# Optimization experiments

Measured on AMD Instinct MI355X. Metric: run time of the kernel, lower is better.

## Reference

```python
import jax, jax.numpy as jnp
import numpy as np

D, H, L, P, NQ, B, DFF = 256, 8, 4, 5, 900, 8, 1024
DH = D // H
SHAPES = np.array([[128, 128], [64, 64], [32, 32], [16, 16]], dtype=np.int64)
S = int((SHAPES[:, 0] * SHAPES[:, 1]).sum())  # 21760
EPS = 1e-5


def layer_norm(x, g, b):
    m = jnp.mean(x, -1, keepdims=True)
    v = jnp.mean((x - m) ** 2, -1, keepdims=True)
    return (x - m) * jax.lax.rsqrt(v + EPS) * g + b


def bilerp(v2, x, y, Wl, Hl):
    # v2: [BH, Hl, Wl, Dh]; x, y: [BH, N] pixel coords (align_corners=False)
    x0 = jnp.floor(x); y0 = jnp.floor(y)
    fx = x - x0; fy = y - y0
    x0i = x0.astype(jnp.int32); y0i = y0.astype(jnp.int32)
    bidx = jnp.arange(v2.shape[0])[:, None]
    out = jnp.zeros(x.shape + (v2.shape[-1],), v2.dtype)
    for dy in (0, 1):
        for dx in (0, 1):
            xi = x0i + dx; yi = y0i + dy
            w = (fx if dx else 1.0 - fx) * (fy if dy else 1.0 - fy)
            valid = (xi >= 0) & (xi < Wl) & (yi >= 0) & (yi < Hl)
            xc = jnp.clip(xi, 0, Wl - 1); yc = jnp.clip(yi, 0, Hl - 1)
            out = out + (w * valid)[..., None] * v2[bidx, yc, xc]
    return out


def setup_inputs() -> dict:
    key = jax.random.key(0)
    ks = jax.random.split(key, 32)
    p = lambda i, shp: (jax.random.normal(ks[i], shp, jnp.float32) * 0.02)
    inp = {
        'tgt': jax.random.normal(ks[0], (NQ, B, D), jnp.float32),
        'tgt_query_pos': jax.random.normal(ks[1], (NQ, B, D), jnp.float32),
        'tgt_reference_points': jax.random.uniform(ks[2], (NQ, B, L, 4), jnp.float32),
        'memory': jax.random.normal(ks[3], (S, B, D), jnp.float32),
        'sa_in_w': p(4, (3 * D, D)), 'sa_in_b': jnp.zeros((3 * D,)),
        'sa_out_w': p(5, (D, D)), 'sa_out_b': jnp.zeros((D,)),
        'off_w': p(6, (H * L * P * 2, D)), 'off_b': jax.random.uniform(ks[7], (H * L * P * 2,), jnp.float32, -1.0, 1.0),
        'aw_w': p(8, (H * L * P, D)), 'aw_b': jnp.zeros((H * L * P,)),
        'val_w': p(9, (D, D)), 'val_b': jnp.zeros((D,)),
        'co_w': p(10, (D, D)), 'co_b': jnp.zeros((D,)),
        'w1': p(11, (DFF, D)), 'b1': jnp.zeros((DFF,)),
        'w2': p(12, (D, DFF)), 'b2': jnp.zeros((D,)),
        'ln1_g': jnp.ones((D,)), 'ln1_b': jnp.zeros((D,)),
        'ln2_g': jnp.ones((D,)), 'ln2_b': jnp.zeros((D,)),
        'ln3_g': jnp.ones((D,)), 'ln3_b': jnp.zeros((D,)),
        'memory_spatial_shapes': np.array(SHAPES),
        'memory_level_start_index': np.concatenate([[0], np.cumsum(SHAPES[:, 0] * SHAPES[:, 1])[:-1]]),
    }
    return inp


def reference(tgt, tgt_query_pos, tgt_reference_points, memory,
              sa_in_w, sa_in_b, sa_out_w, sa_out_b,
              off_w, off_b, aw_w, aw_b, val_w, val_b, co_w, co_b,
              w1, b1, w2, b2, ln1_g, ln1_b, ln2_g, ln2_b, ln3_g, ln3_b,
              memory_spatial_shapes, memory_level_start_index):
    shapes = np.asarray(memory_spatial_shapes)

    # ---- self-attention (norm2) ----
    q = tgt + tgt_query_pos  # [nq,B,D], k == q, v == tgt
    qp = (q @ sa_in_w[:D].T + sa_in_b[:D]).reshape(NQ, B, H, DH)
    kp = (q @ sa_in_w[D:2 * D].T + sa_in_b[D:2 * D]).reshape(NQ, B, H, DH)
    vp = (tgt @ sa_in_w[2 * D:].T + sa_in_b[2 * D:]).reshape(NQ, B, H, DH)
    scores = jnp.einsum('qbhd,kbhd->bhqk', qp, kp) / jnp.sqrt(jnp.float32(DH))
    attn = jax.nn.softmax(scores, -1)
    sa = jnp.einsum('bhqk,kbhd->qbhd', attn, vp).reshape(NQ, B, D)
    sa = sa @ sa_out_w.T + sa_out_b
    tgt = layer_norm(tgt + sa, ln2_g, ln2_b)

    # ---- deformable cross-attention (norm1) ----
    query = (tgt + tgt_query_pos).transpose(1, 0, 2)          # [B,nq,D]
    value = (memory.transpose(1, 0, 2) @ val_w.T + val_b).reshape(B, S, H, DH)
    offsets = (query @ off_w.T + off_b).reshape(B, NQ, H, L, P, 2)
    aw = (query @ aw_w.T + aw_b).reshape(B, NQ, H, L * P)
    aw = jax.nn.softmax(aw, -1).reshape(B, NQ, H, L, P)
    ref = tgt_reference_points.transpose(1, 0, 2, 3)          # [B,nq,L,4]
    locs = ref[:, :, None, :, None, :2] + offsets / P * ref[:, :, None, :, None, 2:] * 0.5

    acc = jnp.zeros((B, H, NQ, DH), jnp.float32)
    start = 0
    for l in range(L):
        Hl, Wl = int(shapes[l, 0]), int(shapes[l, 1])
        v2 = value[:, start:start + Hl * Wl].reshape(B, Hl, Wl, H, DH)
        v2 = v2.transpose(0, 3, 1, 2, 4).reshape(B * H, Hl, Wl, DH)
        loc = locs[:, :, :, l].transpose(0, 2, 1, 3, 4).reshape(B * H, NQ * P, 2)
        x = loc[..., 0] * Wl - 0.5
        y = loc[..., 1] * Hl - 0.5
        samp = bilerp(v2, x, y, Wl, Hl).reshape(B, H, NQ, P, DH)
        w_l = aw[:, :, :, l].transpose(0, 2, 1, 3)            # [B,H,nq,P]
        acc = acc + jnp.einsum('bhqp,bhqpd->bhqd', w_l, samp)
        start += Hl * Wl
    ca = acc.transpose(0, 2, 1, 3).reshape(B, NQ, D) @ co_w.T + co_b
    tgt = layer_norm(tgt + ca.transpose(1, 0, 2), ln1_g, ln1_b)

    # ---- FFN (norm3) ----
    h = jax.nn.relu(tgt @ w1.T + b1) @ w2.T + b2
    tgt = layer_norm(tgt + h, ln3_g, ln3_b)
    return tgt
```

## Files before the change

### kernel.cpp

```cpp
#include <hip/hip_runtime.h>
#include <hip/hip_bf16.h>

#define NQ   900
#define BB   8
#define DD   256
#define HH   8
#define DH   32
#define LL   4
#define PP   5
#define SS   21760
#define DFF  1024
#define MQ   (NQ*BB)
#define MV   (SS*BB)

typedef __bf16 bf16_t;
typedef __bf16 bf16x8 __attribute__((ext_vector_type(8)));
typedef __bf16 bf16x4 __attribute__((ext_vector_type(4)));
typedef float  f32x4  __attribute__((ext_vector_type(4)));

__device__ __forceinline__ void async16(const void* g, void* l) {
  __builtin_amdgcn_global_load_lds(
      (const __attribute__((address_space(1))) unsigned int*)g,
      (__attribute__((address_space(3))) unsigned int*)l, 16, 0, 0);
}

template<typename AT, typename OT, int RELU>
__global__ __launch_bounds__(256) void vgemm(
    const AT* __restrict__ A, const bf16_t* __restrict__ W,
    const float* __restrict__ bias, OT* __restrict__ C,
    int M, int N, int nt)
{
  constexpr bool AF = (sizeof(AT) == 4);
  __shared__ __align__(16) bf16_t Ws[64 * 256];
  const int blk = blockIdx.x;
  const int tn = blk % nt, tm = blk / nt;
  const int n0 = tn << 6, m0 = tm << 8;
  const int t = threadIdx.x, wave = t >> 6, lane = t & 63;
  const int lm = lane & 15, quad = lane >> 4;

#pragma unroll
  for (int j = 0; j < 8; ++j) {
    int flat = j * 4096 + t * 16;
    int col = flat >> 9;
    int kc = ((flat >> 4) & 31) ^ (col & 31);
    int colg = n0 + col; if (colg >= N) colg = N - 1;
    async16(&W[(size_t)colg * 256 + kc * 8], (char*)Ws + flat);
  }
  __syncthreads();

  f32x4 acc[4][4];
#pragma unroll
  for (int i = 0; i < 4; ++i)
#pragma unroll
    for (int j = 0; j < 4; ++j) acc[i][j] = (f32x4){0.f, 0.f, 0.f, 0.f};

#pragma unroll 2
  for (int k0 = 0; k0 < 256; k0 += 32) {
    const int ki = k0 >> 3;
    bf16x8 bfr[4];
#pragma unroll
    for (int ni = 0; ni < 4; ++ni) {
      int col = ni * 16 + lm;
      int ch = (ki + quad) ^ (col & 31);
      bfr[ni] = *(const bf16x8*)&Ws[col * 256 + ch * 8];
    }
    bf16x8 af[4];
#pragma unroll
    for (int mi = 0; mi < 4; ++mi) {
      int row = m0 + wave * 64 + mi * 16 + lm; if (row >= M) row = M - 1;
      if constexpr (AF) {
        const float* ap = A + (size_t)row * 256 + k0 + quad * 8;
        f32x4 lo = *(const f32x4*)ap;
        f32x4 hi = *(const f32x4*)(ap + 4);
        bf16x8 f;
#pragma unroll
        for (int j = 0; j < 4; ++j) { f[j] = (bf16_t)lo[j]; f[4 + j] = (bf16_t)hi[j]; }
        af[mi] = f;
      } else {
        af[mi] = *(const bf16x8*)&A[(size_t)row * 256 + k0 + quad * 8];
      }
    }
#pragma unroll
    for (int mi = 0; mi < 4; ++mi)
#pragma unroll
      for (int ni = 0; ni < 4; ++ni)
        acc[mi][ni] = __builtin_amdgcn_mfma_f32_16x16x32_bf16(af[mi], bfr[ni], acc[mi][ni], 0, 0, 0);
  }

  float bv[4];
#pragma unroll
  for (int ni = 0; ni < 4; ++ni) {
    int c = n0 + ni * 16 + lm;
    bv[ni] = (c < N) ? bias[c] : 0.f;
  }

  if constexpr (sizeof(OT) == 4) {
#pragma unroll
    for (int mi = 0; mi < 4; ++mi) {
#pragma unroll
      for (int r = 0; r < 4; ++r) {
        int row = m0 + wave * 64 + mi * 16 + quad * 4 + r;
        if (row < M) {
#pragma unroll
          for (int ni = 0; ni < 4; ++ni) {
            int col = n0 + ni * 16 + lm;
            if (col < N) {
              float v = acc[mi][ni][r] + bv[ni];
              if (RELU) v = fmaxf(v, 0.f);
              C[(size_t)row * N + col] = (OT)v;
            }
          }
        }
      }
    }
  } else {
    __syncthreads();
    bf16_t* Os = Ws;
#pragma unroll
    for (int mi = 0; mi < 4; ++mi)
#pragma unroll
      for (int r = 0; r < 4; ++r) {
        int rl = wave * 64 + mi * 16 + quad * 4 + r;
#pragma unroll
        for (int ni = 0; ni < 4; ++ni) {
          float v = acc[mi][ni][r] + bv[ni];
          if (RELU) v = fmaxf(v, 0.f);
          Os[rl * 64 + ni * 16 + lm] = (bf16_t)v;
        }
      }
    __syncthreads();
#pragma unroll
    for (int i = 0; i < 8; ++i) {
      int fe = i * 2048 + t * 8;
      int rl = fe >> 6, cl = fe & 63;
      int row = m0 + rl, colg = n0 + cl;
      if (row < M && colg < N)
        *(bf16x8*)&C[(size_t)row * N + colg] = *(const bf16x8*)&Os[fe];
    }
  }
}

template<typename AT, int EPI, typename OT>
__global__ __launch_bounds__(256) void gemm128(
    const AT* __restrict__ A, const bf16_t* __restrict__ W,
    const float* __restrict__ bias, OT* __restrict__ C,
    int M, int N, int K, int tiles_n)
{
  __shared__ __align__(16) bf16_t As[128 * 32];
  __shared__ __align__(16) bf16_t Bs[128 * 32];
  const int tm = blockIdx.x / tiles_n;
  const int tn = blockIdx.x - tm * tiles_n;
  const int m0 = tm << 7, n0 = tn << 7;
  const int t = threadIdx.x;
  const int wave = t >> 6, lane = t & 63;
  const int wr = wave >> 1, wc = wave & 1;
  const int lm = lane & 15, kq = lane >> 4;

  f32x4 acc[4][4];
#pragma unroll
  for (int i = 0; i < 4; ++i)
#pragma unroll
    for (int j = 0; j < 4; ++j) acc[i][j] = (f32x4){0.f, 0.f, 0.f, 0.f};

  for (int k0 = 0; k0 < K; k0 += 32) {
    __syncthreads();
#pragma unroll
    for (int i = 0; i < 2; ++i) {
      int flat = i * 4096 + t * 16;
      int row = flat >> 6;
      int cl = (flat >> 4) & 3;
      int cg = cl ^ ((row >> 1) & 3);
      int grow = m0 + row; if (grow >= M) grow = M - 1;
      async16(&A[(size_t)grow * K + k0 + cg * 8], (char*)As + flat);
    }
#pragma unroll
    for (int i = 0; i < 2; ++i) {
      int flat = i * 4096 + t * 16;
      int row = flat >> 6;
      int cl = (flat >> 4) & 3;
      int cg = cl ^ ((row >> 1) & 3);
      int grow = n0 + row; if (grow >= N) grow = N - 1;
      async16(&W[(size_t)grow * K + k0 + cg * 8], (char*)Bs + flat);
    }
    __syncthreads();

    bf16x8 af[4], bfr[4];
#pragma unroll
    for (int mi = 0; mi < 4; ++mi) {
      int row = wr * 64 + mi * 16 + lm;
      int s = (row >> 1) & 3;
      af[mi] = *(const bf16x8*)((const bf16_t*)As + row * 32 + ((kq ^ s) << 3));
    }
#pragma unroll
    for (int ni = 0; ni < 4; ++ni) {
      int row = wc * 64 + ni * 16 + lm;
      int s = (row >> 1) & 3;
      bfr[ni] = *(const bf16x8*)(Bs + row * 32 + ((kq ^ s) << 3));
    }
#pragma unroll
    for (int mi = 0; mi < 4; ++mi)
#pragma unroll
      for (int ni = 0; ni < 4; ++ni)
        acc[mi][ni] = __builtin_amdgcn_mfma_f32_16x16x32_bf16(af[mi], bfr[ni], acc[mi][ni], 0, 0, 0);
  }

  const int colb = n0 + wc * 64 + lm;
  float bv[4]; bool cok[4];
#pragma unroll
  for (int ni = 0; ni < 4; ++ni) {
    int c = colb + ni * 16;
    cok[ni] = (c < N);
    bv[ni] = cok[ni] ? bias[c] : 0.f;
  }
#pragma unroll
  for (int mi = 0; mi < 4; ++mi) {
    int rbase = m0 + wr * 64 + mi * 16 + kq * 4;
#pragma unroll
    for (int reg = 0; reg < 4; ++reg) {
      int r = rbase + reg;
      if (r < M) {
#pragma unroll
        for (int ni = 0; ni < 4; ++ni) if (cok[ni]) {
          float v = acc[mi][ni][reg] + bv[ni];
          if (EPI == 1) v = fmaxf(v, 0.f);
          C[(size_t)r * N + colb + ni * 16] = (OT)v;
        }
      }
    }
  }
}

__global__ __launch_bounds__(256) void cvt_all(
    const float* __restrict__ s0, const float* __restrict__ s1,
    const float* __restrict__ s2, const float* __restrict__ s3,
    const float* __restrict__ s4, const float* __restrict__ s5,
    const float* __restrict__ s6, const float* __restrict__ s7,
    bf16_t* __restrict__ dst)
{
  int i = blockIdx.x * 256 + threadIdx.x;
  if (i >= 130048) return;
  const float* s; int base;
  if (i < 24576)      { s = s0; base = 0; }
  else if (i < 32768) { s = s1; base = 24576; }
  else if (i < 43008) { s = s2; base = 32768; }
  else if (i < 48128) { s = s3; base = 43008; }
  else if (i < 56320) { s = s4; base = 48128; }
  else if (i < 64512) { s = s5; base = 56320; }
  else if (i < 97280) { s = s6; base = 64512; }
  else                { s = s7; base = 97280; }
  int li = i - base;
  f32x4 x0 = ((const f32x4*)s)[2 * li], x1 = ((const f32x4*)s)[2 * li + 1];
  bf16x8 r;
#pragma unroll
  for (int j = 0; j < 4; ++j) { r[j] = (bf16_t)x0[j]; r[4 + j] = (bf16_t)x1[j]; }
  ((bf16x8*)dst)[i] = r;
}

__global__ __launch_bounds__(256) void addpos_kernel(
    const float* __restrict__ a, const float* __restrict__ b,
    bf16_t* __restrict__ o, int n8)
{
  int i = blockIdx.x * 256 + threadIdx.x;
  if (i < n8) {
    f32x4 x0 = ((const f32x4*)a)[2 * i], x1 = ((const f32x4*)a)[2 * i + 1];
    f32x4 y0 = ((const f32x4*)b)[2 * i], y1 = ((const f32x4*)b)[2 * i + 1];
    bf16x8 r;
#pragma unroll
    for (int j = 0; j < 4; ++j) { r[j] = (bf16_t)(x0[j] + y0[j]); r[4 + j] = (bf16_t)(x1[j] + y1[j]); }
    ((bf16x8*)o)[i] = r;
  }
}

template<int WBF>
__global__ __launch_bounds__(256) void lnres_kernel(
    const float* __restrict__ x, const float* __restrict__ res,
    const float* __restrict__ g, const float* __restrict__ bta,
    float* __restrict__ out, bf16_t* __restrict__ outb, int rows)
{
  int wave = threadIdx.x >> 6, lane = threadIdx.x & 63;
  int row = blockIdx.x * 4 + wave;
  if (row >= rows) return;
  const float4* xp = (const float4*)(x + (size_t)row * DD);
  const float4* rp = (const float4*)(res + (size_t)row * DD);
  float4 v = xp[lane], rr = rp[lane];
  float a0 = v.x + rr.x, a1 = v.y + rr.y, a2 = v.z + rr.z, a3 = v.w + rr.w;
  float s = a0 + a1 + a2 + a3;
#pragma unroll
  for (int off = 32; off; off >>= 1) s += __shfl_xor(s, off);
  float mean = s * (1.0f / DD);
  float d0 = a0 - mean, d1 = a1 - mean, d2 = a2 - mean, d3 = a3 - mean;
  float vs = d0 * d0 + d1 * d1 + d2 * d2 + d3 * d3;
#pragma unroll
  for (int off = 32; off; off >>= 1) vs += __shfl_xor(vs, off);
  float inv = rsqrtf(vs * (1.0f / DD) + 1e-5f);
  float4 gg = ((const float4*)g)[lane];
  float4 bb = ((const float4*)bta)[lane];
  float o0 = d0 * inv * gg.x + bb.x, o1 = d1 * inv * gg.y + bb.y;
  float o2 = d2 * inv * gg.z + bb.z, o3 = d3 * inv * gg.w + bb.w;
  float4 o; o.x = o0; o.y = o1; o.z = o2; o.w = o3;
  ((float4*)(out + (size_t)row * DD))[lane] = o;
  if (WBF) {
    bf16x4 ob; ob[0] = (bf16_t)o0; ob[1] = (bf16_t)o1; ob[2] = (bf16_t)o2; ob[3] = (bf16_t)o3;
    ((bf16x4*)(outb + (size_t)row * DD))[lane] = ob;
  }
}

__global__ __launch_bounds__(256) void attn_mfma(
    const bf16_t* __restrict__ qk, const bf16_t* __restrict__ vp,
    bf16_t* __restrict__ sa)
{
  __shared__ __align__(16) bf16_t Ks[128 * 32];
  __shared__ __align__(16) bf16_t VT[32 * 136];
  __shared__ __align__(16) bf16_t Pw[4][16 * 136];
  const int bh = blockIdx.x;
  const int b = bh & 7, h = bh >> 3;
  const int qt = blockIdx.y;
  const int t = threadIdx.x, wave = t >> 6, lane = t & 63;
  const int lm = lane & 15, quad = lane >> 4;
  const int q0 = qt * 64 + wave * 16;

  int qrow = q0 + lm; if (qrow > NQ - 1) qrow = NQ - 1;
  bf16x8 aqr = *(const bf16x8*)&qk[((size_t)qrow * BB + b) * 512 + h * 32 + quad * 8];
  bf16x8 aq;
#pragma unroll
  for (int j = 0; j < 8; ++j) aq[j] = (bf16_t)((float)aqr[j] * 0.17677669529663687f);

  f32x4 m_run = {-1e30f, -1e30f, -1e30f, -1e30f};
  f32x4 l_run = {0.f, 0.f, 0.f, 0.f};
  f32x4 o0 = {0.f, 0.f, 0.f, 0.f}, o1 = {0.f, 0.f, 0.f, 0.f};
  const f32x4 zero = {0.f, 0.f, 0.f, 0.f};

  for (int c = 0; c < 8; ++c) {
    const int k0 = c * 128;
    __syncthreads();
#pragma unroll
    for (int i = 0; i < 2; ++i) {
      int flat = i * 4096 + t * 16;
      int row = flat >> 6;
      int cl = (flat >> 4) & 3;
      int cg = cl ^ ((row >> 1) & 3);
      int key = k0 + row; if (key > NQ - 1) key = NQ - 1;
      async16(&qk[((size_t)key * BB + b) * 512 + 256 + h * 32 + cg * 8], (char*)Ks + flat);
    }
#pragma unroll
    for (int i = 0; i < 2; ++i) {
      int idx = t * 2 + i;
      int key = idx >> 2, dc = idx & 3;
      int gk = k0 + key;
      if (gk < NQ) {
        bf16x8 vv = *(const bf16x8*)&vp[((size_t)gk * BB + b) * 256 + h * 32 + dc * 8];
#pragma unroll
        for (int u = 0; u < 8; ++u) VT[(dc * 8 + u) * 136 + key] = vv[u];
      } else {
#pragma unroll
        for (int u = 0; u < 8; ++u) VT[(dc * 8 + u) * 136 + key] = (bf16_t)0.f;
      }
    }
    __syncthreads();

    f32x4 s[8];
#pragma unroll
    for (int blk = 0; blk < 8; ++blk) {
      int row = blk * 16 + lm;
      int sw = (row >> 1) & 3;
      bf16x8 kb = *(const bf16x8*)&Ks[row * 32 + ((quad ^ sw) << 3)];
      s[blk] = __builtin_amdgcn_mfma_f32_16x16x32_bf16(aq, kb, zero, 0, 0, 0);
    }
    if (c == 7) {
#pragma unroll
      for (int blk = 0; blk < 8; ++blk) {
        if (k0 + blk * 16 + lm >= NQ) {
#pragma unroll
          for (int r = 0; r < 4; ++r) s[blk][r] = -1e30f;
        }
      }
    }
    f32x4 mx = s[0];
#pragma unroll
    for (int blk = 1; blk < 8; ++blk)
#pragma unroll
      for (int r = 0; r < 4; ++r) mx[r] = fmaxf(mx[r], s[blk][r]);
#pragma unroll
    for (int d = 1; d < 16; d <<= 1)
#pragma unroll
      for (int r = 0; r < 4; ++r) mx[r] = fmaxf(mx[r], __shfl_xor(mx[r], d));
    f32x4 m_new, alpha;
#pragma unroll
    for (int r = 0; r < 4; ++r) {
      m_new[r] = fmaxf(m_run[r], mx[r]);
      alpha[r] = __expf(m_run[r] - m_new[r]);
    }
    f32x4 psum = {0.f, 0.f, 0.f, 0.f};
#pragma unroll
    for (int blk = 0; blk < 8; ++blk) {
#pragma unroll
      for (int r = 0; r < 4; ++r) {
        float p = __expf(s[blk][r] - m_new[r]);
        psum[r] += p;
        Pw[wave][(quad * 4 + r) * 136 + blk * 16 + lm] = (bf16_t)p;
      }
    }
#pragma unroll
    for (int d = 1; d < 16; d <<= 1)
#pragma unroll
      for (int r = 0; r < 4; ++r) psum[r] += __shfl_xor(psum[r], d);
#pragma unroll
    for (int r = 0; r < 4; ++r) {
      l_run[r] = l_run[r] * alpha[r] + psum[r];
      m_run[r] = m_new[r];
      o0[r] *= alpha[r];
      o1[r] *= alpha[r];
    }
    bf16x8 ap[4];
#pragma unroll
    for (int kc = 0; kc < 4; ++kc)
      ap[kc] = *(const bf16x8*)&Pw[wave][lm * 136 + kc * 32 + quad * 8];
#pragma unroll
    for (int kc = 0; kc < 4; ++kc) {
      bf16x8 vb0 = *(const bf16x8*)&VT[lm * 136 + kc * 32 + quad * 8];
      bf16x8 vb1 = *(const bf16x8*)&VT[(16 + lm) * 136 + kc * 32 + quad * 8];
      o0 = __builtin_amdgcn_mfma_f32_16x16x32_bf16(ap[kc], vb0, o0, 0, 0, 0);
      o1 = __builtin_amdgcn_mfma_f32_16x16x32_bf16(ap[kc], vb1, o1, 0, 0, 0);
    }
  }
#pragma unroll
  for (int r = 0; r < 4; ++r) {
    int q = q0 + quad * 4 + r;
    if (q < NQ) {
      float inv = 1.0f / l_run[r];
      size_t base = ((size_t)q * BB + b) * 256 + h * 32;
      sa[base + lm] = (bf16_t)(o0[r] * inv);
      sa[base + 16 + lm] = (bf16_t)(o1[r] * inv);
    }
  }
}

__global__ __launch_bounds__(256) void deform_kernel(
    const bf16_t* __restrict__ value, const float* __restrict__ offs,
    const float* __restrict__ awl, const float* __restrict__ refp,
    bf16_t* __restrict__ out)
{
  __shared__ float logits[160];
  __shared__ float wfin[160][4];
  __shared__ int   tidx[160][4];
  __shared__ float hmax[8], hsum[8];
  const int r = blockIdx.x;
  const int b = r & 7;
  const int t = threadIdx.x;
  if (t < 160) {
    int i20 = t % 20;
    int l = i20 / 5;
    logits[t] = awl[(size_t)r * 160 + t];
    float ox = offs[(size_t)r * 320 + t * 2];
    float oy = offs[(size_t)r * 320 + t * 2 + 1];
    const float* rp = refp + ((size_t)r * LL + l) * 4;
    int Wl = 128 >> l;
    int st = (l == 0) ? 0 : (l == 1) ? 16384 : (l == 2) ? 20480 : 21504;
    float lx = rp[0] + ox * 0.1f * rp[2];
    float ly = rp[1] + oy * 0.1f * rp[3];
    float xx = lx * (float)Wl - 0.5f;
    float yy = ly * (float)Wl - 0.5f;
    float x0f = floorf(xx), y0f = floorf(yy);
    float fx = xx - x0f, fy = yy - y0f;
    int x0 = (int)x0f, y0 = (int)y0f;
#pragma unroll
    for (int tap = 0; tap < 4; ++tap) {
      int dx = tap & 1, dy = tap >> 1;
      int xi = x0 + dx, yi = y0 + dy;
      float w = (dx ? fx : 1.0f - fx) * (dy ? fy : 1.0f - fy);
      bool valid = (xi >= 0) & (xi < Wl) & (yi >= 0) & (yi < Wl);
      int xc = min(max(xi, 0), Wl - 1);
      int yc = min(max(yi, 0), Wl - 1);
      tidx[t][tap] = (st + yc * Wl + xc) * BB + b;
      wfin[t][tap] = valid ? w : 0.0f;
    }
  }
  __syncthreads();
  if (t < 8) {
    float m = -1e30f;
    for (int i = 0; i < 20; ++i) m = fmaxf(m, logits[t * 20 + i]);
    float s = 0.f;
    for (int i = 0; i < 20; ++i) s += __expf(logits[t * 20 + i] - m);
    hmax[t] = m; hsum[t] = s;
  }
  __syncthreads();
  if (t < 160) {
    int h = t / 20;
    float p = __expf(logits[t] - hmax[h]) / hsum[h];
#pragma unroll
    for (int tap = 0; tap < 4; ++tap) wfin[t][tap] *= p;
  }
  __syncthreads();
  const int h = t >> 5, d = t & 31;
  const bf16_t* vbase = value + h * 32 + d;
  float acc = 0.f;
#pragma unroll 4
  for (int i = 0; i < 20; ++i) {
    int e = h * 20 + i;
#pragma unroll
    for (int tap = 0; tap < 4; ++tap) {
      float w = wfin[e][tap];
      float v = (float)vbase[(size_t)tidx[e][tap] * 256];
      acc = fmaf(w, v, acc);
    }
  }
  out[(size_t)r * 256 + t] = (bf16_t)acc;
}

static inline int tiles(int x) { return (x + 127) >> 7; }

extern "C" void kernel_launch(void* const* d_in, const int* in_sizes, int n_in,
                              void* d_out, int out_size, void* d_ws, size_t ws_size,
                              hipStream_t stream) {
  const float* tgt     = (const float*)d_in[0];
  const float* pos     = (const float*)d_in[1];
  const float* refp    = (const float*)d_in[2];
  const float* memory  = (const float*)d_in[3];
  const float* sa_in_w = (const float*)d_in[4];
  const float* sa_in_b = (const float*)d_in[5];
  const float* sa_out_w= (const float*)d_in[6];
  const float* sa_out_b= (const float*)d_in[7];
  const float* off_w   = (const float*)d_in[8];
  const float* off_b   = (const float*)d_in[9];
  const float* aw_w    = (const float*)d_in[10];
  const float* aw_b    = (const float*)d_in[11];
  const float* val_w   = (const float*)d_in[12];
  const float* val_b   = (const float*)d_in[13];
  const float* co_w    = (const float*)d_in[14];
  const float* co_b    = (const float*)d_in[15];
  const float* w1      = (const float*)d_in[16];
  const float* b1      = (const float*)d_in[17];
  const float* w2      = (const float*)d_in[18];
  const float* b2      = (const float*)d_in[19];
  const float* ln1_g   = (const float*)d_in[20];
  const float* ln1_b   = (const float*)d_in[21];
  const float* ln2_g   = (const float*)d_in[22];
  const float* ln2_b   = (const float*)d_in[23];
  const float* ln3_g   = (const float*)d_in[24];
  const float* ln3_b   = (const float*)d_in[25];

  char* ws = (char*)d_ws;
  bf16_t* value_bf = (bf16_t*)ws;
  bf16_t* qk_bf    = (bf16_t*)(ws + 89128960);
  bf16_t* h1_bf    = qk_bf;
  bf16_t* qsum_bf  = (bf16_t*)(ws + 103874560);
  bf16_t* vp_bf    = (bf16_t*)(ws + 107560960);
  bf16_t* sa_bf    = (bf16_t*)(ws + 111247360);
  float*  tgt2     = (float*)(ws + 114933760);
  bf16_t* query_bf = (bf16_t*)(ws + 122306560);
  float*  offs     = (float*)(ws + 125992960);
  float*  awl      = (float*)(ws + 135208960);
  bf16_t* ca_bf    = (bf16_t*)(ws + 139816960);
  float*  gout     = (float*)(ws + 143503360);
  float*  tgt3     = (float*)(ws + 150876160);
  bf16_t* tgt3_bf  = (bf16_t*)(ws + 158248960);
  bf16_t* wbf      = (bf16_t*)(ws + 161935360);
  bf16_t* sa_in_wb = wbf;
  bf16_t* sa_out_wb= wbf + 196608;
  bf16_t* off_wb   = wbf + 262144;
  bf16_t* aw_wb    = wbf + 344064;
  bf16_t* val_wb   = wbf + 385024;
  bf16_t* co_wb    = wbf + 450560;
  bf16_t* w1b      = wbf + 516096;
  bf16_t* w2b      = wbf + 778240;
  float*  outp     = (float*)d_out;

  const int n8q = MQ * DD / 8;
  const int mtq = (MQ + 255) >> 8;

  cvt_all<<<dim3(508), 256, 0, stream>>>(
      sa_in_w, sa_out_w, off_w, aw_w, val_w, co_w, w1, w2, wbf);

  addpos_kernel<<<dim3((n8q + 255) / 256), 256, 0, stream>>>(tgt, pos, qsum_bf, n8q);
  vgemm<bf16_t, bf16_t, 0><<<dim3(mtq * 8), 256, 0, stream>>>(
      qsum_bf, sa_in_wb, sa_in_b, qk_bf, MQ, 512, 8);
  vgemm<float, bf16_t, 0><<<dim3(mtq * 4), 256, 0, stream>>>(
      tgt, sa_in_wb + 512 * 256, sa_in_b + 512, vp_bf, MQ, 256, 4);
  attn_mfma<<<dim3(64, 15), 256, 0, stream>>>(qk_bf, vp_bf, sa_bf);
  vgemm<bf16_t, float, 0><<<dim3(mtq * 4), 256, 0, stream>>>(
      sa_bf, sa_out_wb, sa_out_b, gout, MQ, 256, 4);
  lnres_kernel<0><<<dim3((MQ + 3) / 4), 256, 0, stream>>>(
      gout, tgt, ln2_g, ln2_b, tgt2, (bf16_t*)nullptr, MQ);

  addpos_kernel<<<dim3((n8q + 255) / 256), 256, 0, stream>>>(tgt2, pos, query_bf, n8q);
  vgemm<float, bf16_t, 0><<<dim3(680 * 4), 256, 0, stream>>>(
      memory, val_wb, val_b, value_bf, MV, 256, 4);
  vgemm<bf16_t, float, 0><<<dim3(mtq * 5), 256, 0, stream>>>(
      query_bf, off_wb, off_b, offs, MQ, 320, 5);
  vgemm<bf16_t, float, 0><<<dim3(mtq * 3), 256, 0, stream>>>(
      query_bf, aw_wb, aw_b, awl, MQ, 160, 3);
  deform_kernel<<<dim3(MQ), 256, 0, stream>>>(value_bf, offs, awl, refp, ca_bf);
  vgemm<bf16_t, float, 0><<<dim3(mtq * 4), 256, 0, stream>>>(
      ca_bf, co_wb, co_b, gout, MQ, 256, 4);
  lnres_kernel<1><<<dim3((MQ + 3) / 4), 256, 0, stream>>>(
      gout, tgt2, ln1_g, ln1_b, tgt3, tgt3_bf, MQ);

  vgemm<bf16_t, bf16_t, 1><<<dim3(mtq * 16), 256, 0, stream>>>(
      tgt3_bf, w1b, b1, h1_bf, MQ, 1024, 16);
  gemm128<bf16_t, 0, float><<<dim3(tiles(MQ) * 2), 256, 0, stream>>>(
      h1_bf, w2b, b2, gout, MQ, 256, DFF, 2);
  lnres_kernel<0><<<dim3((MQ + 3) / 4), 256, 0, stream>>>(
      gout, tgt3, ln3_g, ln3_b, outp, (bf16_t*)nullptr, MQ);

  (void)in_sizes; (void)n_in; (void)out_size; (void)ws_size;
}
```

Measured before the change: 608.7 us.

## Fuse offset and attention-weight projections; swizzle and nontemporal-store value GEMM

Merges the sampling-offset and attention-logit projections into one 480-column GEMM. The weights were already contiguous, and a concatenated bias buffer is now built in the weight-conversion kernel. The deform kernel reads both from the combined buffer, which saves a launch and a second read of the query activations. The large value-projection GEMM gets a block-index swizzle that groups 8 M-tiles sharing each weight N-tile, and it now writes its output with nontemporal stores to avoid polluting the cache. The 480-wide GEMM uses 8 N-tiles of 64 (512 columns), so some weight rows are clamped and their output is masked off, which wastes some work.

```diff
diff --git a/kernel.cpp b/kernel.cpp
--- a/kernel.cpp
+++ b/kernel.cpp
@@ -24,7 +24,7 @@
       (__attribute__((address_space(3))) unsigned int*)l, 16, 0, 0);
 }
 
-template<typename AT, typename OT, int RELU>
+template<typename AT, typename OT, int RELU, int SWZ, int NT>
 __global__ __launch_bounds__(256) void vgemm(
     const AT* __restrict__ A, const bf16_t* __restrict__ W,
     const float* __restrict__ bias, OT* __restrict__ C,
@@ -32,8 +32,15 @@
 {
   constexpr bool AF = (sizeof(AT) == 4);
   __shared__ __align__(16) bf16_t Ws[64 * 256];
-  const int blk = blockIdx.x;
-  const int tn = blk % nt, tm = blk / nt;
+  int tn, tm;
+  if (SWZ) {
+    int u = blockIdx.x >> 3;
+    tn = u % nt;
+    tm = (u / nt) * 8 + (blockIdx.x & 7);
+  } else {
+    tn = blockIdx.x % nt;
+    tm = blockIdx.x / nt;
+  }
   const int n0 = tn << 6, m0 = tm << 8;
   const int t = threadIdx.x, wave = t >> 6, lane = t & 63;
   const int lm = lane & 15, quad = lane >> 4;
@@ -134,8 +141,11 @@
       int fe = i * 2048 + t * 8;
       int rl = fe >> 6, cl = fe & 63;
       int row = m0 + rl, colg = n0 + cl;
-      if (row < M && colg < N)
-        *(bf16x8*)&C[(size_t)row * N + colg] = *(const bf16x8*)&Os[fe];
+      if (row < M && colg < N) {
+        bf16x8 v8 = *(const bf16x8*)&Os[fe];
+        if (NT) __builtin_nontemporal_store(v8, (bf16x8*)&C[(size_t)row * N + colg]);
+        else *(bf16x8*)&C[(size_t)row * N + colg] = v8;
+      }
     }
   }
 }
@@ -235,25 +245,31 @@
     const float* __restrict__ s2, const float* __restrict__ s3,
     const float* __restrict__ s4, const float* __restrict__ s5,
     const float* __restrict__ s6, const float* __restrict__ s7,
-    bf16_t* __restrict__ dst)
+    bf16_t* __restrict__ dst,
+    const float* __restrict__ ob, const float* __restrict__ ab,
+    float* __restrict__ bcat)
 {
   int i = blockIdx.x * 256 + threadIdx.x;
-  if (i >= 130048) return;
-  const float* s; int base;
-  if (i < 24576)      { s = s0; base = 0; }
-  else if (i < 32768) { s = s1; base = 24576; }
-  else if (i < 43008) { s = s2; base = 32768; }
-  else if (i < 48128) { s = s3; base = 43008; }
-  else if (i < 56320) { s = s4; base = 48128; }
-  else if (i < 64512) { s = s5; base = 56320; }
-  else if (i < 97280) { s = s6; base = 64512; }
-  else                { s = s7; base = 97280; }
-  int li = i - base;
-  f32x4 x0 = ((const f32x4*)s)[2 * li], x1 = ((const f32x4*)s)[2 * li + 1];
-  bf16x8 r;
-#pragma unroll
-  for (int j = 0; j < 4; ++j) { r[j] = (bf16_t)x0[j]; r[4 + j] = (bf16_t)x1[j]; }
-  ((bf16x8*)dst)[i] = r;
+  if (i < 130048) {
+    const float* s; int base;
+    if (i < 24576)      { s = s0; base = 0; }
+    else if (i < 32768) { s = s1; base = 24576; }
+    else if (i < 43008) { s = s2; base = 32768; }
+    else if (i < 48128) { s = s3; base = 43008; }
+    else if (i < 56320) { s = s4; base = 48128; }
+    else if (i < 64512) { s = s5; base = 56320; }
+    else if (i < 97280) { s = s6; base = 64512; }
+    else                { s = s7; base = 97280; }
+    int li = i - base;
+    f32x4 x0 = ((const f32x4*)s)[2 * li], x1 = ((const f32x4*)s)[2 * li + 1];
+    bf16x8 r;
+#pragma unroll
+    for (int j = 0; j < 4; ++j) { r[j] = (bf16_t)x0[j]; r[4 + j] = (bf16_t)x1[j]; }
+    ((bf16x8*)dst)[i] = r;
+  } else {
+    int j = i - 130048;
+    if (j < 480) bcat[j] = (j < 320) ? ob[j] : ab[j - 320];
+  }
 }
 
 __global__ __launch_bounds__(256) void addpos_kernel(
@@ -436,9 +452,8 @@
 }
 
 __global__ __launch_bounds__(256) void deform_kernel(
-    const bf16_t* __restrict__ value, const float* __restrict__ offs,
-    const float* __restrict__ awl, const float* __restrict__ refp,
-    bf16_t* __restrict__ out)
+    const bf16_t* __restrict__ value, const float* __restrict__ oa,
+    const float* __restrict__ refp, bf16_t* __restrict__ out)
 {
   __shared__ float logits[160];
   __shared__ float wfin[160][4];
@@ -450,9 +465,9 @@
   if (t < 160) {
     int i20 = t % 20;
     int l = i20 / 5;
-    logits[t] = awl[(size_t)r * 160 + t];
-    float ox = offs[(size_t)r * 320 + t * 2];
-    float oy = offs[(size_t)r * 320 + t * 2 + 1];
+    logits[t] = oa[(size_t)r * 480 + 320 + t];
+    float ox = oa[(size_t)r * 480 + t * 2];
+    float oy = oa[(size_t)r * 480 + t * 2 + 1];
     const float* rp = refp + ((size_t)r * LL + l) * 4;
     int Wl = 128 >> l;
     int st = (l == 0) ? 0 : (l == 1) ? 16384 : (l == 2) ? 20480 : 21504;
@@ -548,8 +563,7 @@
   bf16_t* sa_bf    = (bf16_t*)(ws + 111247360);
   float*  tgt2     = (float*)(ws + 114933760);
   bf16_t* query_bf = (bf16_t*)(ws + 122306560);
-  float*  offs     = (float*)(ws + 125992960);
-  float*  awl      = (float*)(ws + 135208960);
+  float*  oa       = (float*)(ws + 125992960);
   bf16_t* ca_bf    = (bf16_t*)(ws + 139816960);
   float*  gout     = (float*)(ws + 143503360);
   float*  tgt3     = (float*)(ws + 150876160);
@@ -557,45 +571,44 @@
   bf16_t* wbf      = (bf16_t*)(ws + 161935360);
   bf16_t* sa_in_wb = wbf;
   bf16_t* sa_out_wb= wbf + 196608;
-  bf16_t* off_wb   = wbf + 262144;
-  bf16_t* aw_wb    = wbf + 344064;
+  bf16_t* oa_wb    = wbf + 262144;
   bf16_t* val_wb   = wbf + 385024;
   bf16_t* co_wb    = wbf + 450560;
   bf16_t* w1b      = wbf + 516096;
   bf16_t* w2b      = wbf + 778240;
+  float*  oabias   = (float*)(ws + 164016128);
   float*  outp     = (float*)d_out;
 
   const int n8q = MQ * DD / 8;
   const int mtq = (MQ + 255) >> 8;
 
-  cvt_all<<<dim3(508), 256, 0, stream>>>(
-      sa_in_w, sa_out_w, off_w, aw_w, val_w, co_w, w1, w2, wbf);
+  cvt_all<<<dim3(510), 256, 0, stream>>>(
+      sa_in_w, sa_out_w, off_w, aw_w, val_w, co_w, w1, w2, wbf,
+      off_b, aw_b, oabias);
 
   addpos_kernel<<<dim3((n8q + 255) / 256), 256, 0, stream>>>(tgt, pos, qsum_bf, n8q);
-  vgemm<bf16_t, bf16_t, 0><<<dim3(mtq * 8), 256, 0, stream>>>(
+  vgemm<bf16_t, bf16_t, 0, 0, 0><<<dim3(mtq * 8), 256, 0, stream>>>(
       qsum_bf, sa_in_wb, sa_in_b, qk_bf, MQ, 512, 8);
-  vgemm<float, bf16_t, 0><<<dim3(mtq * 4), 256, 0, stream>>>(
+  vgemm<float, bf16_t, 0, 0, 0><<<dim3(mtq * 4), 256, 0, stream>>>(
       tgt, sa_in_wb + 512 * 256, sa_in_b + 512, vp_bf, MQ, 256, 4);
   attn_mfma<<<dim3(64, 15), 256, 0, stream>>>(qk_bf, vp_bf, sa_bf);
-  vgemm<bf16_t, float, 0><<<dim3(mtq * 4), 256, 0, stream>>>(
+  vgemm<bf16_t, float, 0, 0, 0><<<dim3(mtq * 4), 256, 0, stream>>>(
       sa_bf, sa_out_wb, sa_out_b, gout, MQ, 256, 4);
   lnres_kernel<0><<<dim3((MQ + 3) / 4), 256, 0, stream>>>(
       gout, tgt, ln2_g, ln2_b, tgt2, (bf16_t*)nullptr, MQ);
 
   addpos_kernel<<<dim3((n8q + 255) / 256), 256, 0, stream>>>(tgt2, pos, query_bf, n8q);
-  vgemm<float, bf16_t, 0><<<dim3(680 * 4), 256, 0, stream>>>(
+  vgemm<float, bf16_t, 0, 1, 1><<<dim3(680 * 4), 256, 0, stream>>>(
       memory, val_wb, val_b, value_bf, MV, 256, 4);
-  vgemm<bf16_t, float, 0><<<dim3(mtq * 5), 256, 0, stream>>>(
-      query_bf, off_wb, off_b, offs, MQ, 320, 5);
-  vgemm<bf16_t, float, 0><<<dim3(mtq * 3), 256, 0, stream>>>(
-      query_bf, aw_wb, aw_b, awl, MQ, 160, 3);
-  deform_kernel<<<dim3(MQ), 256, 0, stream>>>(value_bf, offs, awl, refp, ca_bf);
-  vgemm<bf16_t, float, 0><<<dim3(mtq * 4), 256, 0, stream>>>(
+  vgemm<bf16_t, float, 0, 0, 0><<<dim3(mtq * 8), 256, 0, stream>>>(
+      query_bf, oa_wb, oabias, oa, MQ, 480, 8);
+  deform_kernel<<<dim3(MQ), 256, 0, stream>>>(value_bf, oa, refp, ca_bf);
+  vgemm<bf16_t, float, 0, 0, 0><<<dim3(mtq * 4), 256, 0, stream>>>(
       ca_bf, co_wb, co_b, gout, MQ, 256, 4);
   lnres_kernel<1><<<dim3((MQ + 3) / 4), 256, 0, stream>>>(
       gout, tgt2, ln1_g, ln1_b, tgt3, tgt3_bf, MQ);
 
-  vgemm<bf16_t, bf16_t, 1><<<dim3(mtq * 16), 256, 0, stream>>>(
+  vgemm<bf16_t, bf16_t, 1, 0, 0><<<dim3(mtq * 16), 256, 0, stream>>>(
       tgt3_bf, w1b, b1, h1_bf, MQ, 1024, 16);
   gemm128<bf16_t, 0, float><<<dim3(tiles(MQ) * 2), 256, 0, stream>>>(
       h1_bf, w2b, b2, gout, MQ, 256, DFF, 2);
```

Result: faster. 584.7 us (-3.9%).
